# Kernel optimization log

Hardware: AMD Instinct MI355X
Metric: run time of the kernel (lower is better)

## Reference

```python
import jax, jax.numpy as jnp
import numpy as np
import math

D_MODEL = 1024
N_HEADS = 16
D_K = D_MODEL // N_HEADS
HIDDEN = 4096
R_SOFTPLUS_0 = 1.442695041
EPS = 1e-6


def setup_inputs() -> dict:
    key = jax.random.key(0)
    ks = jax.random.split(key, 16)
    B, S = 4, 2048
    s = 0.02
    inp = {
        "inputs": jax.random.normal(ks[0], (B, S, D_MODEL), jnp.float32),
        "mask": jnp.zeros((1, 1, S, S), jnp.float32),
        # RmsNorm (direct_scale=True -> init 1.0)
        "rms_scale": jnp.ones((D_MODEL,), jnp.float32),
        # attention projections (torch Linear: y = x @ W.T + b)
        "Wq": jax.random.normal(ks[1], (D_MODEL, D_MODEL), jnp.float32) * s,
        "bq": jnp.zeros((D_MODEL,), jnp.float32),
        "Wk": jax.random.normal(ks[2], (D_MODEL, D_MODEL), jnp.float32) * s,
        "bk": jnp.zeros((D_MODEL,), jnp.float32),
        "Wv": jax.random.normal(ks[3], (D_MODEL, D_MODEL), jnp.float32) * s,
        "bv": jnp.zeros((D_MODEL,), jnp.float32),
        "per_dim_scale": jnp.zeros((D_K,), jnp.float32),
        "Wpost": jax.random.normal(ks[4], (D_MODEL, D_MODEL), jnp.float32) * s,
        "bpost": jnp.zeros((D_MODEL,), jnp.float32),
        # FFN LayerNorm (direct_scale=False -> scale param init 0, effective 1+scale)
        "ln_scale": jnp.zeros((D_MODEL,), jnp.float32),
        "ln_bias": jnp.zeros((D_MODEL,), jnp.float32),
        "W1": jax.random.normal(ks[5], (HIDDEN, D_MODEL), jnp.float32) * s,
        "b1": jnp.zeros((HIDDEN,), jnp.float32),
        "W2": jax.random.normal(ks[6], (D_MODEL, HIDDEN), jnp.float32) * s,
        "b2": jnp.zeros((D_MODEL,), jnp.float32),
    }
    return inp


def _rms_norm(x, scale):
    ms = jnp.mean(x * x, axis=-1, keepdims=True)
    return x * jax.lax.rsqrt(ms + EPS) * scale


def _layer_norm(x, scale, bias):
    mean = jnp.mean(x, axis=-1, keepdims=True)
    var = jnp.mean((x - mean) ** 2, axis=-1, keepdims=True)
    return (x - mean) * jax.lax.rsqrt(var + EPS) * (1.0 + scale) + bias


def reference(inputs, mask, rms_scale, Wq, bq, Wk, bk, Wv, bv, per_dim_scale,
              Wpost, bpost, ln_scale, ln_bias, W1, b1, W2, b2):
    B, S, _ = inputs.shape
    x = _rms_norm(inputs, rms_scale)
    # projections -> [B, H, S, Dk]
    def split_heads(t):
        return t.reshape(B, S, N_HEADS, D_K).transpose(0, 2, 1, 3)
    q = split_heads(x @ Wq.T + bq)
    k = split_heads(x @ Wk.T + bk)
    v = split_heads(x @ Wv.T + bv)
    # PerDimScale: (r_softplus_0 / sqrt(d_k)) * softplus(param)
    scale = (R_SOFTPLUS_0 / math.sqrt(D_K)) * jax.nn.softplus(per_dim_scale)
    q = q * scale
    attn = jnp.einsum("bhqd,bhkd->bhqk", q, k) + mask
    attn = jax.nn.softmax(attn, axis=-1)
    out = jnp.einsum("bhqk,bhkd->bhqd", attn, v)
    out = out.transpose(0, 2, 1, 3).reshape(B, S, D_MODEL)
    attn_out = out @ Wpost.T + bpost
    h = attn_out + inputs  # residual (dropout=0)
    # FeedForward with pre-LayerNorm and residual
    y = _layer_norm(h, ln_scale, ln_bias)
    y = jax.nn.relu(y @ W1.T + b1)
    y = y @ W2.T + b2
    return y + h
```

## Files before the change

### kernel.cpp

```cpp
#include <hip/hip_runtime.h>
#include <hip/hip_bf16.h>

typedef unsigned short u16;
typedef __attribute__((ext_vector_type(8))) short short8;
typedef __attribute__((ext_vector_type(4))) float floatx4;

#define R_PDS 0.18033688f
#define LOG2E 1.4426950408889634f

__device__ __forceinline__ float bf2f(u16 u) {
    union { float f; unsigned int i; } c; c.i = ((unsigned int)u) << 16; return c.f;
}
__device__ __forceinline__ u16 f2b(float f) {
    union { float f; unsigned int i; } c; c.f = f;
    unsigned int r = c.i + 0x7fffu + ((c.i >> 16) & 1u);
    return (u16)(r >> 16);
}
__device__ __forceinline__ unsigned int pk2(float a, float b) {
    __hip_bfloat162 h = __float22bfloat162_rn(float2{a, b});
    unsigned int u; __builtin_memcpy(&u, &h, 4); return u;
}

__device__ __forceinline__ void async16(const u16* g, u16* l) {
    __builtin_amdgcn_global_load_lds(
        (const __attribute__((address_space(1))) unsigned int*)g,
        (__attribute__((address_space(3))) unsigned int*)l, 16, 0, 0);
}

__global__ __launch_bounds__(256) void f2b_all_k(const float* __restrict__ Wq, const float* __restrict__ Wk,
                                                 const float* __restrict__ Wv, const float* __restrict__ Wp,
                                                 const float* __restrict__ W1, const float* __restrict__ W2,
                                                 u16* __restrict__ Wqkvb, u16* __restrict__ Wpb,
                                                 u16* __restrict__ W1b,  u16* __restrict__ W2b,
                                                 int* flag) {
    int bid = blockIdx.x;
    if (bid == 0 && threadIdx.x == 0) *flag = 0;
    const float* src; u16* dst; int off;
    if      (bid < 1024) { src = Wq; dst = Wqkvb;                off = bid; }
    else if (bid < 2048) { src = Wk; dst = Wqkvb + 1024 * 1024;  off = bid - 1024; }
    else if (bid < 3072) { src = Wv; dst = Wqkvb + 2048 * 1024;  off = bid - 2048; }
    else if (bid < 4096) { src = Wp; dst = Wpb;                  off = bid - 3072; }
    else if (bid < 8192) { src = W1; dst = W1b;                  off = bid - 4096; }
    else                 { src = W2; dst = W2b;                  off = bid - 8192; }
    int i = off * 256 + threadIdx.x;
    float4 v = ((const float4*)src)[i];
    uint2 w; w.x = pk2(v.x, v.y); w.y = pk2(v.z, v.w);
    ((uint2*)dst)[i] = w;
}

__global__ __launch_bounds__(256) void mask_any_k(const float* __restrict__ mask, int* flag) {
    int i = blockIdx.x * 256 + threadIdx.x;
    uint4 u = ((const uint4*)mask)[i];
    unsigned int v = (u.x | u.y | u.z | u.w) & 0x7fffffffu;
    if (v) atomicOr(flag, 1);
}

__global__ __launch_bounds__(256) void rmsnorm_k(const float* __restrict__ in,
                                                 const float* __restrict__ gscale,
                                                 u16* __restrict__ out) {
    int row = blockIdx.x;
    int t = threadIdx.x, lane = t & 63, wave = t >> 6;
    const float* x = in + (size_t)row * 1024;
    float4 v = *(const float4*)(x + t * 4);
    float ss = v.x*v.x + v.y*v.y + v.z*v.z + v.w*v.w;
    for (int o = 1; o < 64; o <<= 1) ss += __shfl_xor(ss, o, 64);
    __shared__ float red[4];
    if (lane == 0) red[wave] = ss;
    __syncthreads();
    float tot = red[0] + red[1] + red[2] + red[3];
    float inv = rsqrtf(tot * (1.0f / 1024.0f) + 1e-6f);
    float4 s = *(const float4*)(gscale + t * 4);
    uint2 w;
    w.x = pk2(v.x * inv * s.x, v.y * inv * s.y);
    w.y = pk2(v.z * inv * s.z, v.w * inv * s.w);
    *(uint2*)(out + (size_t)row * 1024 + t * 4) = w;
}

__global__ __launch_bounds__(256) void layernorm_k(const u16* __restrict__ in,
                                                   const float* __restrict__ gs,
                                                   const float* __restrict__ gb,
                                                   u16* __restrict__ out) {
    int row = blockIdx.x;
    int t = threadIdx.x, lane = t & 63, wave = t >> 6;
    const u16* x = in + (size_t)row * 1024;
    uint2 u = *(const uint2*)(x + t * 4);
    float v0 = bf2f((u16)(u.x & 0xffff)), v1 = bf2f((u16)(u.x >> 16));
    float v2 = bf2f((u16)(u.y & 0xffff)), v3 = bf2f((u16)(u.y >> 16));
    float s1 = v0 + v1 + v2 + v3;
    float s2 = v0*v0 + v1*v1 + v2*v2 + v3*v3;
    for (int o = 1; o < 64; o <<= 1) { s1 += __shfl_xor(s1, o, 64); s2 += __shfl_xor(s2, o, 64); }
    __shared__ float r1[4], r2[4];
    if (lane == 0) { r1[wave] = s1; r2[wave] = s2; }
    __syncthreads();
    float mean = (r1[0] + r1[1] + r1[2] + r1[3]) * (1.0f / 1024.0f);
    float var  = (r2[0] + r2[1] + r2[2] + r2[3]) * (1.0f / 1024.0f) - mean * mean;
    var = fmaxf(var, 0.0f);
    float inv = rsqrtf(var + 1e-6f);
    float4 sc = *(const float4*)(gs + t * 4);
    float4 bb = *(const float4*)(gb + t * 4);
    uint2 w;
    w.x = pk2((v0 - mean) * inv * (1.0f + sc.x) + bb.x,
              (v1 - mean) * inv * (1.0f + sc.y) + bb.y);
    w.y = pk2((v2 - mean) * inv * (1.0f + sc.z) + bb.z,
              (v3 - mean) * inv * (1.0f + sc.w) + bb.w);
    *(uint2*)(out + (size_t)row * 1024 + t * 4) = w;
}

__device__ __forceinline__ void xcd_swizzle(int& bx, int& by) {
    int gx = gridDim.x, nwg = gx * gridDim.y;
    int lin = blockIdx.y * gx + blockIdx.x;
    int swz = (lin & 7) * (nwg >> 3) + (lin >> 3);
    bx = swz % gx; by = swz / gx;
}

__device__ __forceinline__ void gemm8_core(const u16* __restrict__ A, const u16* __restrict__ B,
                                           int K, int NG, int m0, int n0,
                                           u16* lds, floatx4 (&acc)[8][4]) {
    const int t = threadIdx.x, wave = t >> 6, lane = t & 63;
    const int quad = lane >> 4, ln = lane & 15;
    const int wave_m = wave >> 2, wave_n = wave & 3;

    const int rowS = t >> 3;
    const int srcb = ((t & 7) * 16) ^ (((t >> 3) & 7) << 4);
    const u16* Ab = A + (size_t)(m0 + rowS) * K + (srcb >> 1);
    const u16* Bb = B + (size_t)(n0 + rowS) * K + (srcb >> 1);
    const size_t rstep = (size_t)64 * K;
    const size_t hstep = (size_t)128 * K;
    const int ldw = wave * 512;

    #define STAGE_A8(buf, h, kt) do { \
        u16* _l = lds + (buf) * 32768 + (h) * 8192 + ldw; \
        const u16* _g = Ab + (size_t)(h) * hstep + (kt); \
        async16(_g, _l); async16(_g + rstep, _l + 4096); } while (0)
    #define STAGE_B8(buf, h, kt) do { \
        u16* _l = lds + (buf) * 32768 + 16384 + (h) * 8192 + ldw; \
        const u16* _g = Bb + (size_t)(h) * hstep + (kt); \
        async16(_g, _l); async16(_g + rstep, _l + 4096); } while (0)

    #define RD8(base, lr, ks) \
        (*(const short8*)((base) + (lr) * 64 + ((((ks) * 64 + quad * 16) ^ (((lr) & 7) << 4)) >> 1)))

    STAGE_B8(0, 0, 0); STAGE_B8(0, 1, 0);
    STAGE_A8(0, 0, 0); STAGE_A8(0, 1, 0);
    if (NG > 1) {
        STAGE_B8(1, 0, 64); STAGE_B8(1, 1, 64);
        asm volatile("s_waitcnt vmcnt(4)" ::: "memory");
    } else {
        asm volatile("s_waitcnt vmcnt(0)" ::: "memory");
    }
    __builtin_amdgcn_s_barrier();

    for (int g = 0; g < NG; ++g) {
        const int cur = g & 1;
        const u16* aH = lds + cur * 32768 + wave_m * 8192;
        const u16* bH = lds + cur * 32768 + 16384 + (wave_n >> 1) * 8192;
        const int lrB = (wave_n & 1) * 64;
        short8 bf[4][2];
        #pragma unroll
        for (int q = 0; q < 4; ++q) {
            short8 af[2][2];
            #pragma unroll
            for (int mt = 0; mt < 2; ++mt)
                #pragma unroll
                for (int ks = 0; ks < 2; ++ks)
                    af[mt][ks] = RD8(aH, q * 32 + mt * 16 + ln, ks);
            if (q == 0) {
                #pragma unroll
                for (int nt = 0; nt < 4; ++nt)
                    #pragma unroll
                    for (int ks = 0; ks < 2; ++ks)
                        bf[nt][ks] = RD8(bH, lrB + nt * 16 + ln, ks);
            }
            if (q == 0 && g + 1 < NG) STAGE_A8(cur ^ 1, 0, (g + 1) * 64);
            if (q == 1 && g + 1 < NG) STAGE_A8(cur ^ 1, 1, (g + 1) * 64);
            if (q == 2 && g + 2 < NG) STAGE_B8(cur, 0, (g + 2) * 64);
            if (q == 3 && g + 2 < NG) STAGE_B8(cur, 1, (g + 2) * 64);
            __builtin_amdgcn_s_barrier();
            asm volatile("s_waitcnt lgkmcnt(0)" ::: "memory");
            __builtin_amdgcn_sched_barrier(0);
            __builtin_amdgcn_s_setprio(1);
            #pragma unroll
            for (int ks = 0; ks < 2; ++ks)
                #pragma unroll
                for (int mt = 0; mt < 2; ++mt)
                    #pragma unroll
                    for (int nt = 0; nt < 4; ++nt)
                        acc[q * 2 + mt][nt] = __builtin_amdgcn_mfma_f32_16x16x32_bf16(
                            af[mt][ks], bf[nt][ks], acc[q * 2 + mt][nt], 0, 0, 0);
            __builtin_amdgcn_s_setprio(0);
            __builtin_amdgcn_sched_barrier(0);
            if (q == 3 && g + 1 < NG) {
                if (g + 2 < NG) asm volatile("s_waitcnt vmcnt(4)" ::: "memory");
                else            asm volatile("s_waitcnt vmcnt(0)" ::: "memory");
            }
            __builtin_amdgcn_s_barrier();
        }
    }
    #undef STAGE_A8
    #undef STAGE_B8
    #undef RD8
}

__device__ __forceinline__ void gemm8h_core(const u16* __restrict__ A, const u16* __restrict__ B,
                                            int K, int NG, int m0, int n0,
                                            u16* lds, floatx4 (&acc)[4][4]) {
    const int t = threadIdx.x, wave = t >> 6, lane = t & 63;
    const int quad = lane >> 4, ln = lane & 15;
    const int wm = (wave >> 2) * 64, wn = (wave & 3) * 64;

    const int rowS = t >> 3;
    const int srcb = ((t & 7) * 16) ^ (((t >> 3) & 7) << 4);
    const u16* Ab = A + (size_t)(m0 + rowS) * K + (srcb >> 1);
    const u16* Bb = B + (size_t)(n0 + rowS) * K + (srcb >> 1);
    const size_t hstep = (size_t)64 * K;
    const int ldw = wave * 512;

    #define STAGE_AH(buf, h, kt) \
        async16(Ab + (size_t)(h) * hstep + (kt), lds + (buf) * 24576 + (h) * 4096 + ldw)
    #define STAGE_BH(buf, h, kt) \
        async16(Bb + (size_t)(h) * hstep + (kt), lds + (buf) * 24576 + 8192 + (h) * 4096 + ldw)
    #define RD8H(base, lr, ks) \
        (*(const short8*)((base) + (lr) * 64 + ((((ks) * 64 + quad * 16) ^ (((lr) & 7) << 4)) >> 1)))

    STAGE_BH(0, 0, 0); STAGE_BH(0, 1, 0); STAGE_BH(0, 2, 0); STAGE_BH(0, 3, 0);
    STAGE_AH(0, 0, 0); STAGE_AH(0, 1, 0);
    if (NG > 1) {
        STAGE_BH(1, 0, 64); STAGE_BH(1, 1, 64); STAGE_BH(1, 2, 64); STAGE_BH(1, 3, 64);
        asm volatile("s_waitcnt vmcnt(4)" ::: "memory");
    } else {
        asm volatile("s_waitcnt vmcnt(0)" ::: "memory");
    }
    __builtin_amdgcn_s_barrier();

    for (int g = 0; g < NG; ++g) {
        const int cur = g & 1;
        const u16* aB = lds + cur * 24576;
        const u16* bB = lds + cur * 24576 + 8192;
        short8 bf[4][2];
        #pragma unroll
        for (int q = 0; q < 2; ++q) {
            short8 af[2][2];
            #pragma unroll
            for (int mt = 0; mt < 2; ++mt)
                #pragma unroll
                for (int ks = 0; ks < 2; ++ks)
                    af[mt][ks] = RD8H(aB, wm + (q * 2 + mt) * 16 + ln, ks);
            if (q == 0) {
                #pragma unroll
                for (int nt = 0; nt < 4; ++nt)
                    #pragma unroll
                    for (int ks = 0; ks < 2; ++ks)
                        bf[nt][ks] = RD8H(bB, wn + nt * 16 + ln, ks);
            }
            if (q == 0 && g + 1 < NG) {
                STAGE_AH(cur ^ 1, 0, (g + 1) * 64); STAGE_AH(cur ^ 1, 1, (g + 1) * 64);
            }
            if (q == 1 && g + 2 < NG) {
                STAGE_BH(cur, 0, (g + 2) * 64); STAGE_BH(cur, 1, (g + 2) * 64);
                STAGE_BH(cur, 2, (g + 2) * 64); STAGE_BH(cur, 3, (g + 2) * 64);
            }
            __builtin_amdgcn_s_barrier();
            asm volatile("s_waitcnt lgkmcnt(0)" ::: "memory");
            __builtin_amdgcn_sched_barrier(0);
            __builtin_amdgcn_s_setprio(1);
            #pragma unroll
            for (int ks = 0; ks < 2; ++ks)
                #pragma unroll
                for (int mt = 0; mt < 2; ++mt)
                    #pragma unroll
                    for (int nt = 0; nt < 4; ++nt)
                        acc[q * 2 + mt][nt] = __builtin_amdgcn_mfma_f32_16x16x32_bf16(
                            af[mt][ks], bf[nt][ks], acc[q * 2 + mt][nt], 0, 0, 0);
            __builtin_amdgcn_s_setprio(0);
            __builtin_amdgcn_sched_barrier(0);
            if (q == 1 && g + 1 < NG) {
                if (g + 2 < NG) asm volatile("s_waitcnt vmcnt(4)" ::: "memory");
                else            asm volatile("s_waitcnt vmcnt(0)" ::: "memory");
            }
            __builtin_amdgcn_s_barrier();
        }
    }
    #undef STAGE_AH
    #undef STAGE_BH
    #undef RD8H
}

template <int EPI, bool OUTF32, bool RESF32>
__global__ __launch_bounds__(512, 2) void gemm8_bt_k(const u16* __restrict__ A,
                                                     const u16* __restrict__ B,
                                                     const float* __restrict__ bias,
                                                     const void* __restrict__ res,
                                                     void* __restrict__ Cv,
                                                     int M, int N, int K) {
    __shared__ __align__(16) u16 lds[65536];
    int bx, by; xcd_swizzle(bx, by);
    const int m0 = by * 256, n0 = bx * 256;
    const int t = threadIdx.x, wave = t >> 6, lane = t & 63;
    const int quad = lane >> 4, ln = lane & 15;
    const int wm = (wave >> 2) * 128, wn = (wave & 3) * 64;

    floatx4 acc[8][4];
    #pragma unroll
    for (int mf = 0; mf < 8; mf++)
        #pragma unroll
        for (int nf = 0; nf < 4; nf++) acc[mf][nf] = (floatx4)0.0f;

    gemm8_core(A, B, K, K >> 6, m0, n0, lds, acc);

    #pragma unroll
    for (int nf = 0; nf < 4; nf++) {
        int col = n0 + wn + nf * 16 + ln;
        float bv = bias[col];
        #pragma unroll
        for (int mf = 0; mf < 8; mf++) {
            int row = m0 + wm + mf * 16 + quad * 4;
            #pragma unroll
            for (int r = 0; r < 4; r++) {
                float v = acc[mf][nf][r] + bv;
                if (EPI == 1) v = fmaxf(v, 0.0f);
                if (EPI == 2) {
                    if (RESF32) v += ((const float*)res)[(size_t)(row + r) * N + col];
                    else        v += bf2f(((const u16*)res)[(size_t)(row + r) * N + col]);
                }
                if (OUTF32) ((float*)Cv)[(size_t)(row + r) * N + col] = v;
                else        ((u16*)Cv)[(size_t)(row + r) * N + col] = f2b(v);
            }
        }
    }
}

template <int EPI, bool OUTF32, bool RESF32>
__global__ __launch_bounds__(512, 2) void gemm8h_bt_k(const u16* __restrict__ A,
                                                      const u16* __restrict__ B,
                                                      const float* __restrict__ bias,
                                                      const void* __restrict__ res,
                                                      void* __restrict__ Cv,
                                                      int M, int N, int K) {
    __shared__ __align__(16) u16 lds[49152];
    int bx, by; xcd_swizzle(bx, by);
    const int m0 = by * 128, n0 = bx * 256;
    const int t = threadIdx.x, wave = t >> 6, lane = t & 63;
    const int quad = lane >> 4, ln = lane & 15;
    const int wm = (wave >> 2) * 64, wn = (wave & 3) * 64;

    floatx4 acc[4][4];
    #pragma unroll
    for (int mf = 0; mf < 4; mf++)
        #pragma unroll
        for (int nf = 0; nf < 4; nf++) acc[mf][nf] = (floatx4)0.0f;

    gemm8h_core(A, B, K, K >> 6, m0, n0, lds, acc);

    #pragma unroll
    for (int nf = 0; nf < 4; nf++) {
        int col = n0 + wn + nf * 16 + ln;
        float bv = bias[col];
        #pragma unroll
        for (int mf = 0; mf < 4; mf++) {
            int row = m0 + wm + mf * 16 + quad * 4;
            #pragma unroll
            for (int r = 0; r < 4; r++) {
                float v = acc[mf][nf][r] + bv;
                if (EPI == 1) v = fmaxf(v, 0.0f);
                if (EPI == 2) {
                    if (RESF32) v += ((const float*)res)[(size_t)(row + r) * N + col];
                    else        v += bf2f(((const u16*)res)[(size_t)(row + r) * N + col]);
                }
                if (OUTF32) ((float*)Cv)[(size_t)(row + r) * N + col] = v;
                else        ((u16*)Cv)[(size_t)(row + r) * N + col] = f2b(v);
            }
        }
    }
}

__global__ __launch_bounds__(512, 2) void gemm8h_qkv_k(const u16* __restrict__ A,
                                                       const u16* __restrict__ B,
                                                       const float* __restrict__ bq,
                                                       const float* __restrict__ bk,
                                                       const float* __restrict__ bv,
                                                       const float* __restrict__ pds,
                                                       u16* __restrict__ C) {
    const int K = 1024, N = 3072;
    __shared__ __align__(16) u16 lds[49152];
    int bx, by; xcd_swizzle(bx, by);
    const int m0 = by * 128, n0 = bx * 256;
    const int t = threadIdx.x, wave = t >> 6, lane = t & 63;
    const int quad = lane >> 4, ln = lane & 15;
    const int wm = (wave >> 2) * 64, wn = (wave & 3) * 64;

    floatx4 acc[4][4];
    #pragma unroll
    for (int mf = 0; mf < 4; mf++)
        #pragma unroll
        for (int nf = 0; nf < 4; nf++) acc[mf][nf] = (floatx4)0.0f;

    gemm8h_core(A, B, K, K >> 6, m0, n0, lds, acc);

    #pragma unroll
    for (int nf = 0; nf < 4; nf++) {
        int col = n0 + wn + nf * 16 + ln;
        float bv_, sc = 1.0f;
        if (col < 1024) {
            bv_ = bq[col];
            float xp = pds[col & 63];
            float sp = (xp > 20.0f) ? xp : log1pf(__expf(xp));
            sc = R_PDS * sp * LOG2E;
        } else if (col < 2048) bv_ = bk[col - 1024];
        else                   bv_ = bv[col - 2048];
        #pragma unroll
        for (int mf = 0; mf < 4; mf++) {
            int row = m0 + wm + mf * 16 + quad * 4;
            #pragma unroll
            for (int r = 0; r < 4; r++)
                C[(size_t)(row + r) * N + col] = f2b((acc[mf][nf][r] + bv_) * sc);
        }
    }
}

__global__ __launch_bounds__(256) void transpose_v_k(const u16* __restrict__ qkv, u16* __restrict__ vT) {
    __shared__ u16 tile[64][65];
    int st = blockIdx.x, bh = blockIdx.y;
    int b = bh >> 4, h = bh & 15;
    const u16* vb = qkv + (size_t)(b * 2048 + st * 64) * 3072 + 2048 + h * 64;
    int t = threadIdx.x;
    for (int i = t; i < 4096; i += 256) {
        int s = i >> 6, d = i & 63;
        tile[s][d] = vb[(size_t)s * 3072 + d];
    }
    __syncthreads();
    u16* ob = vT + (size_t)bh * 131072 + st * 64;
    for (int i = t; i < 4096; i += 256) {
        int d = i >> 6, s = i & 63;
        ob[(size_t)d * 2048 + s] = tile[s][d];
    }
}

__global__ __launch_bounds__(256, 4) void attn_k(const u16* __restrict__ qkv,
                                                 const u16* __restrict__ vT,
                                                 const float* __restrict__ mask,
                                                 const int* __restrict__ flag,
                                                 u16* __restrict__ o) {
    __shared__ __align__(16) u16 Ksh[4096];
    __shared__ __align__(16) u16 Vsh[4096];
    __shared__ __align__(16) u16 Ps[4096];

    const int t = threadIdx.x, wave = t >> 6, lane = t & 63;
    const int quad = lane >> 4, ln = lane & 15;
    const int lin = blockIdx.y * 16 + blockIdx.x;
    const int qt = (lin >> 3) & 15;
    const int bh = ((lin & 7) << 3) | (lin >> 7);
    const int b = bh >> 4, h = bh & 15;
    const int q0 = qt * 128;
    const int wm = wave * 32;

    const u16* qb = qkv + (size_t)(b * 2048 + q0) * 3072 + h * 64;
    short8 qf[2][2];
    #pragma unroll
    for (int mt = 0; mt < 2; mt++)
        #pragma unroll
        for (int ks = 0; ks < 2; ks++)
            qf[mt][ks] = *(const short8*)(qb + (size_t)(wm + mt * 16 + ln) * 3072 + ks * 32 + quad * 8);

    const int swzK = (ln & 7) << 4;
    const int swzP = (ln & 3) << 4;
    const int o_kA0 = ln * 128 + ((quad * 16) ^ swzK);
    const int o_kA1 = ln * 128 + ((64 + quad * 16) ^ swzK);
    const int o_pv  = ln * 64 + ((quad * 16) ^ swzP);
    const int o_pw0 = wave * 2048 + ln * 64 + ((quad * 8) ^ swzP);
    const int o_pw1 = wave * 2048 + ln * 64 + ((32 + quad * 8) ^ swzP);
    const int o_pr  = wave * 2048 + o_pv;

    #define RD8AT(arr, byteoff) (*(const short8*)((const char*)(arr) + (byteoff)))

    const int rK = t >> 3, sK = (((t & 7) ^ (rK & 7))) * 8;
    const int rV = t >> 2, sV = (((t & 3) ^ (rV & 3))) * 8;
    const u16* kgp = qkv + (size_t)(b * 2048) * 3072 + 1024 + h * 64 + (size_t)rK * 3072 + sK;
    const u16* vgp = vT + (size_t)bh * 131072 + (size_t)rV * 2048 + sV;
    const size_t KADV = (size_t)32 * 3072;

    #define STAGE(c, tile) do { \
        async16(kgp + (size_t)(tile) * KADV, Ksh + (c) * 2048 + t * 8); \
        async16(vgp + (size_t)(tile) * 32,   Vsh + (c) * 2048 + t * 8); } while (0)

    short8 ones_f;
    #pragma unroll
    for (int i = 0; i < 8; i++) ones_f[i] = (short)0x3F80;

    floatx4 acc_o[2][4], acc_l[2];
    #pragma unroll
    for (int mt = 0; mt < 2; mt++) {
        acc_l[mt] = (floatx4)0.0f;
        #pragma unroll
        for (int dt = 0; dt < 4; dt++) acc_o[mt][dt] = (floatx4)0.0f;
    }

    const int mflag = *flag;
    int kvbase = 0;

    STAGE(0, 0);
    STAGE(1, 1);
    asm volatile("s_waitcnt vmcnt(2)" ::: "memory");
    __builtin_amdgcn_s_barrier();

    #define COMPUTE(BUF) do {                                                              \
                           \
        _Pragma("unroll")                                                                  \
        for (int nt = 0; nt < 2; nt++) {                                                   \
            short8 kf0 = RD8AT(Ksh, (BUF) * 4096 + nt * 2048 + o_kA0);                     \
            short8 kf1 = RD8AT(Ksh, (BUF) * 4096 + nt * 2048 + o_kA1);                     \
            floatx4 sa0 = (floatx4)0.0f, sa1 = (floatx4)0.0f;                              \
            sa0 = __builtin_amdgcn_mfma_f32_16x16x32_bf16(kf0, qf[0][0], sa0, 0, 0, 0);    \
            sa0 = __builtin_amdgcn_mfma_f32_16x16x32_bf16(kf1, qf[0][1], sa0, 0, 0, 0);    \
            sa1 = __builtin_amdgcn_mfma_f32_16x16x32_bf16(kf0, qf[1][0], sa1, 0, 0, 0);    \
            sa1 = __builtin_amdgcn_mfma_f32_16x16x32_bf16(kf1, qf[1][1], sa1, 0, 0, 0);    \
            if (mflag) {                                                                   \
                _Pragma("unroll")                                                          \
                for (int r = 0; r < 4; r++) {                                              \
                    int kc = kvbase + nt * 16 + quad * 4 + r;                              \
                    sa0[r] += mask[(size_t)(q0 + wm + ln) * 2048 + kc] * LOG2E;            \
                    sa1[r] += mask[(size_t)(q0 + wm + 16 + ln) * 2048 + kc] * LOG2E;       \
                }                                                                          \
            }                                                                              \
            {                                                                              \
                uint2 w;                                                                   \
                w.x = pk2(__builtin_amdgcn_exp2f(fminf(sa0[0], 80.0f)),                    \
                          __builtin_amdgcn_exp2f(fminf(sa0[1], 80.0f)));                   \
                w.y = pk2(__builtin_amdgcn_exp2f(fminf(sa0[2], 80.0f)),                    \
                          __builtin_amdgcn_exp2f(fminf(sa0[3], 80.0f)));                   \
                *(uint2*)((char*)Ps + (nt ? o_pw1 : o_pw0)) = w;                           \
            }                                                                              \
            {                                                                              \
                uint2 w;                                                                   \
                w.x = pk2(__builtin_amdgcn_exp2f(fminf(sa1[0], 80.0f)),                    \
                          __builtin_amdgcn_exp2f(fminf(sa1[1], 80.0f)));                   \
                w.y = pk2(__builtin_amdgcn_exp2f(fminf(sa1[2], 80.0f)),                    \
                          __builtin_amdgcn_exp2f(fminf(sa1[3], 80.0f)));                   \
                *(uint2*)((char*)Ps + (nt ? o_pw1 : o_pw0) + 1024) = w;                    \
            }                                                                              \
        }                                                                                  \
                                     \
        {                                                                                  \
            short8 vf0 = RD8AT(Vsh, (BUF) * 4096 + 0 * 1024 + o_pv);                       \
            short8 vf1 = RD8AT(Vsh, (BUF) * 4096 + 1 * 1024 + o_pv);                       \
            short8 vf2 = RD8AT(Vsh, (BUF) * 4096 + 2 * 1024 + o_pv);                       \
            short8 vf3 = RD8AT(Vsh, (BUF) * 4096 + 3 * 1024 + o_pv);                       \
            _Pragma("unroll")                                                              \
            for (int mt = 0; mt < 2; mt++) {                                               \
                short8 a = RD8AT(Ps, o_pr + mt * 1024);                                    \
                acc_l[mt] = __builtin_amdgcn_mfma_f32_16x16x32_bf16(a, ones_f, acc_l[mt], 0, 0, 0); \
                acc_o[mt][0] = __builtin_amdgcn_mfma_f32_16x16x32_bf16(a, vf0, acc_o[mt][0], 0, 0, 0); \
                acc_o[mt][1] = __builtin_amdgcn_mfma_f32_16x16x32_bf16(a, vf1, acc_o[mt][1], 0, 0, 0); \
                acc_o[mt][2] = __builtin_amdgcn_mfma_f32_16x16x32_bf16(a, vf2, acc_o[mt][2], 0, 0, 0); \
                acc_o[mt][3] = __builtin_amdgcn_mfma_f32_16x16x32_bf16(a, vf3, acc_o[mt][3], 0, 0, 0); \
            }                                                                              \
        }                                                                                  \
    } while (0)

    #pragma unroll 1
    for (int it = 0; it < 32; ++it) {
        COMPUTE(0);
        __builtin_amdgcn_s_barrier();
        if (it < 31) {
            STAGE(0, 2 * it + 2);
            asm volatile("s_waitcnt vmcnt(2)" ::: "memory");
        } else {
            asm volatile("s_waitcnt vmcnt(0)" ::: "memory");
        }
        __builtin_amdgcn_s_barrier();
        kvbase += 32;
        COMPUTE(1);
        __builtin_amdgcn_s_barrier();
        if (it < 31) {
            STAGE(1, 2 * it + 3);
            asm volatile("s_waitcnt vmcnt(2)" ::: "memory");
        } else {
            asm volatile("s_waitcnt vmcnt(0)" ::: "memory");
        }
        __builtin_amdgcn_s_barrier();
        kvbase += 32;
    }
    #undef COMPUTE
    #undef STAGE
    #undef RD8AT

    u16* ob = o + (size_t)(b * 2048 + q0) * 1024 + h * 64;
    #pragma unroll
    for (int mt = 0; mt < 2; mt++) {
        #pragma unroll
        for (int r = 0; r < 4; r++) {
            float inv = 1.0f / acc_l[mt][r];
            int row = wm + mt * 16 + quad * 4 + r;
            #pragma unroll
            for (int dt = 0; dt < 4; dt++)
                ob[(size_t)row * 1024 + dt * 16 + ln] = f2b(acc_o[mt][dt][r] * inv);
        }
    }
}

extern "C" void kernel_launch(void* const* d_in, const int* in_sizes, int n_in,
                              void* d_out, int out_size, void* d_ws, size_t ws_size,
                              hipStream_t stream) {
    const float* inp    = (const float*)d_in[0];
    const float* mask   = (const float*)d_in[1];
    const float* rms_s  = (const float*)d_in[2];
    const float* Wq     = (const float*)d_in[3];
    const float* bq     = (const float*)d_in[4];
    const float* Wk     = (const float*)d_in[5];
    const float* bk     = (const float*)d_in[6];
    const float* Wv     = (const float*)d_in[7];
    const float* bv     = (const float*)d_in[8];
    const float* pds    = (const float*)d_in[9];
    const float* Wpost  = (const float*)d_in[10];
    const float* bpost  = (const float*)d_in[11];
    const float* ln_s   = (const float*)d_in[12];
    const float* ln_b   = (const float*)d_in[13];
    const float* W1     = (const float*)d_in[14];
    const float* b1     = (const float*)d_in[15];
    const float* W2     = (const float*)d_in[16];
    const float* b2     = (const float*)d_in[17];
    float* out = (float*)d_out;

    char* w = (char*)d_ws;
    const size_t MB = 1u << 20;
    u16* W1b   = (u16*)(w + 0 * MB);
    u16* W2b   = (u16*)(w + 8 * MB);
    u16* qkv   = (u16*)(w + 16 * MB);
    u16* x     = (u16*)(w + 64 * MB);
    u16* o     = (u16*)(w + 64 * MB);
    u16* Wqkvb = (u16*)(w + 80 * MB);
    u16* Wpb   = (u16*)(w + 86 * MB);
    u16* yln   = (u16*)(w + 80 * MB);
    u16* vT    = (u16*)(w + 96 * MB);
    u16* hb    = (u16*)(w + 96 * MB);
    u16* f1    = (u16*)(w + 16 * MB);
    int* flag  = (int*)(w + 112 * MB);

    f2b_all_k<<<12288, 256, 0, stream>>>(Wq, Wk, Wv, Wpost, W1, W2, Wqkvb, Wpb, W1b, W2b, flag);
    mask_any_k<<<4096, 256, 0, stream>>>(mask, flag);

    rmsnorm_k<<<8192, 256, 0, stream>>>(inp, rms_s, x);

    gemm8h_qkv_k<<<dim3(12, 64), 512, 0, stream>>>(x, Wqkvb, bq, bk, bv, pds, qkv);

    transpose_v_k<<<dim3(32, 64), 256, 0, stream>>>(qkv, vT);

    attn_k<<<dim3(16, 64), 256, 0, stream>>>(qkv, vT, mask, flag, o);

    gemm8h_bt_k<2, false, true><<<dim3(4, 64), 512, 0, stream>>>(o, Wpb, bpost, inp, hb, 8192, 1024, 1024);

    layernorm_k<<<8192, 256, 0, stream>>>(hb, ln_s, ln_b, yln);

    gemm8_bt_k<1, false, true><<<dim3(16, 32), 512, 0, stream>>>(yln, W1b, b1, nullptr, f1, 8192, 4096, 1024);
    gemm8h_bt_k<2, true, false><<<dim3(4, 64), 512, 0, stream>>>(f1, W2b, b2, hb, out, 8192, 1024, 4096);
}
```

Baseline: 518.7 us.

## Fuse mask check into RMSNorm, write V transposed from QKV GEMM, widen attention KV tile

Merges the mask-nonzero scan into the RMSNorm launch as extra blocks. The QKV GEMM epilogue now writes V directly into the transposed per-head layout, which removes the separate transpose kernel and its round trip through memory. The attention kernel's KV tile grows from 32 to 64 per stage, with larger LDS buffers and occupancy lowered from 4 to 3 blocks per CU. This means fewer iterations and barriers, at the cost of occupancy and scattered 8-byte V stores.

```diff
diff --git a/kernel.cpp b/kernel.cpp
--- a/kernel.cpp
+++ b/kernel.cpp
@@ -48,23 +48,25 @@
     ((uint2*)dst)[i] = w;
 }
 
-__global__ __launch_bounds__(256) void mask_any_k(const float* __restrict__ mask, int* flag) {
-    int i = blockIdx.x * 256 + threadIdx.x;
-    uint4 u = ((const uint4*)mask)[i];
-    unsigned int v = (u.x | u.y | u.z | u.w) & 0x7fffffffu;
-    if (v) atomicOr(flag, 1);
-}
-
-__global__ __launch_bounds__(256) void rmsnorm_k(const float* __restrict__ in,
-                                                 const float* __restrict__ gscale,
-                                                 u16* __restrict__ out) {
-    int row = blockIdx.x;
+__global__ __launch_bounds__(256) void rms_mask_k(const float* __restrict__ in,
+                                                  const float* __restrict__ gscale,
+                                                  u16* __restrict__ out,
+                                                  const float* __restrict__ mask,
+                                                  int* flag) {
+    __shared__ float red[4];
+    int bid = blockIdx.x;
     int t = threadIdx.x, lane = t & 63, wave = t >> 6;
-    const float* x = in + (size_t)row * 1024;
+    if (bid >= 8192) {
+        int i = (bid - 8192) * 256 + t;
+        uint4 u = ((const uint4*)mask)[i];
+        unsigned int v = (u.x | u.y | u.z | u.w) & 0x7fffffffu;
+        if (v) atomicOr(flag, 1);
+        return;
+    }
+    const float* x = in + (size_t)bid * 1024;
     float4 v = *(const float4*)(x + t * 4);
     float ss = v.x*v.x + v.y*v.y + v.z*v.z + v.w*v.w;
     for (int o = 1; o < 64; o <<= 1) ss += __shfl_xor(ss, o, 64);
-    __shared__ float red[4];
     if (lane == 0) red[wave] = ss;
     __syncthreads();
     float tot = red[0] + red[1] + red[2] + red[3];
@@ -73,7 +75,7 @@
     uint2 w;
     w.x = pk2(v.x * inv * s.x, v.y * inv * s.y);
     w.y = pk2(v.z * inv * s.z, v.w * inv * s.w);
-    *(uint2*)(out + (size_t)row * 1024 + t * 4) = w;
+    *(uint2*)(out + (size_t)bid * 1024 + t * 4) = w;
 }
 
 __global__ __launch_bounds__(256) void layernorm_k(const u16* __restrict__ in,
@@ -379,7 +381,8 @@
                                                        const float* __restrict__ bk,
                                                        const float* __restrict__ bv,
                                                        const float* __restrict__ pds,
-                                                       u16* __restrict__ C) {
+                                                       u16* __restrict__ C,
+                                                       u16* __restrict__ vTout) {
     const int K = 1024, N = 3072;
     __shared__ __align__(16) u16 lds[49152];
     int bx, by; xcd_swizzle(bx, by);
@@ -399,50 +402,49 @@
     #pragma unroll
     for (int nf = 0; nf < 4; nf++) {
         int col = n0 + wn + nf * 16 + ln;
-        float bv_, sc = 1.0f;
-        if (col < 1024) {
-            bv_ = bq[col];
-            float xp = pds[col & 63];
-            float sp = (xp > 20.0f) ? xp : log1pf(__expf(xp));
-            sc = R_PDS * sp * LOG2E;
-        } else if (col < 2048) bv_ = bk[col - 1024];
-        else                   bv_ = bv[col - 2048];
-        #pragma unroll
-        for (int mf = 0; mf < 4; mf++) {
-            int row = m0 + wm + mf * 16 + quad * 4;
-            #pragma unroll
-            for (int r = 0; r < 4; r++)
-                C[(size_t)(row + r) * N + col] = f2b((acc[mf][nf][r] + bv_) * sc);
-        }
-    }
-}
-
-__global__ __launch_bounds__(256) void transpose_v_k(const u16* __restrict__ qkv, u16* __restrict__ vT) {
-    __shared__ u16 tile[64][65];
-    int st = blockIdx.x, bh = blockIdx.y;
-    int b = bh >> 4, h = bh & 15;
-    const u16* vb = qkv + (size_t)(b * 2048 + st * 64) * 3072 + 2048 + h * 64;
-    int t = threadIdx.x;
-    for (int i = t; i < 4096; i += 256) {
-        int s = i >> 6, d = i & 63;
-        tile[s][d] = vb[(size_t)s * 3072 + d];
-    }
-    __syncthreads();
-    u16* ob = vT + (size_t)bh * 131072 + st * 64;
-    for (int i = t; i < 4096; i += 256) {
-        int d = i >> 6, s = i & 63;
-        ob[(size_t)d * 2048 + s] = tile[s][d];
-    }
-}
-
-__global__ __launch_bounds__(256, 4) void attn_k(const u16* __restrict__ qkv,
+        if (col < 2048) {
+            float bv_, sc = 1.0f;
+            if (col < 1024) {
+                bv_ = bq[col];
+                float xp = pds[col & 63];
+                float sp = (xp > 20.0f) ? xp : log1pf(__expf(xp));
+                sc = R_PDS * sp * LOG2E;
+            } else bv_ = bk[col - 1024];
+            #pragma unroll
+            for (int mf = 0; mf < 4; mf++) {
+                int row = m0 + wm + mf * 16 + quad * 4;
+                #pragma unroll
+                for (int r = 0; r < 4; r++)
+                    C[(size_t)(row + r) * N + col] = f2b((acc[mf][nf][r] + bv_) * sc);
+            }
+        } else {
+            float bv_ = bv[col - 2048];
+            int hh = (col - 2048) >> 6, dd = (col - 2048) & 63;
+            #pragma unroll
+            for (int mf = 0; mf < 4; mf++) {
+                int row = m0 + wm + mf * 16 + quad * 4;
+                int bb = row >> 11, ss = row & 2047;
+                u16 u0 = f2b(acc[mf][nf][0] + bv_);
+                u16 u1 = f2b(acc[mf][nf][1] + bv_);
+                u16 u2 = f2b(acc[mf][nf][2] + bv_);
+                u16 u3 = f2b(acc[mf][nf][3] + bv_);
+                uint2 w;
+                w.x = (unsigned int)u0 | ((unsigned int)u1 << 16);
+                w.y = (unsigned int)u2 | ((unsigned int)u3 << 16);
+                *(uint2*)(vTout + (size_t)(bb * 16 + hh) * 131072 + (size_t)dd * 2048 + ss) = w;
+            }
+        }
+    }
+}
+
+__global__ __launch_bounds__(256, 3) void attn_k(const u16* __restrict__ qkv,
                                                  const u16* __restrict__ vT,
                                                  const float* __restrict__ mask,
                                                  const int* __restrict__ flag,
                                                  u16* __restrict__ o) {
-    __shared__ __align__(16) u16 Ksh[4096];
-    __shared__ __align__(16) u16 Vsh[4096];
-    __shared__ __align__(16) u16 Ps[4096];
+    __shared__ __align__(16) u16 Ksh[8192];
+    __shared__ __align__(16) u16 Vsh[8192];
+    __shared__ __align__(16) u16 Ps[8192];
 
     const int t = threadIdx.x, wave = t >> 6, lane = t & 63;
     const int quad = lane >> 4, ln = lane & 15;
@@ -461,26 +463,28 @@
         for (int ks = 0; ks < 2; ks++)
             qf[mt][ks] = *(const short8*)(qb + (size_t)(wm + mt * 16 + ln) * 3072 + ks * 32 + quad * 8);
 
-    const int swzK = (ln & 7) << 4;
-    const int swzP = (ln & 3) << 4;
-    const int o_kA0 = ln * 128 + ((quad * 16) ^ swzK);
-    const int o_kA1 = ln * 128 + ((64 + quad * 16) ^ swzK);
-    const int o_pv  = ln * 64 + ((quad * 16) ^ swzP);
-    const int o_pw0 = wave * 2048 + ln * 64 + ((quad * 8) ^ swzP);
-    const int o_pw1 = wave * 2048 + ln * 64 + ((32 + quad * 8) ^ swzP);
-    const int o_pr  = wave * 2048 + o_pv;
+    const int swz = (ln & 7) << 4;
+    const int o_f0 = ln * 128 + ((quad * 16) ^ swz);
+    const int o_f1 = ln * 128 + ((64 + quad * 16) ^ swz);
+    const int o_q0 = (wm + ln) * 128 + ((quad * 16) ^ swz);
+    const int o_q1 = (wm + ln) * 128 + ((64 + quad * 16) ^ swz);
+    int o_p[4];
+    #pragma unroll
+    for (int nt = 0; nt < 4; nt++)
+        o_p[nt] = (wm + ln) * 128 + ((nt * 32 + quad * 8) ^ swz);
 
     #define RD8AT(arr, byteoff) (*(const short8*)((const char*)(arr) + (byteoff)))
 
-    const int rK = t >> 3, sK = (((t & 7) ^ (rK & 7))) * 8;
-    const int rV = t >> 2, sV = (((t & 3) ^ (rV & 3))) * 8;
-    const u16* kgp = qkv + (size_t)(b * 2048) * 3072 + 1024 + h * 64 + (size_t)rK * 3072 + sK;
-    const u16* vgp = vT + (size_t)bh * 131072 + (size_t)rV * 2048 + sV;
-    const size_t KADV = (size_t)32 * 3072;
-
-    #define STAGE(c, tile) do { \
-        async16(kgp + (size_t)(tile) * KADV, Ksh + (c) * 2048 + t * 8); \
-        async16(vgp + (size_t)(tile) * 32,   Vsh + (c) * 2048 + t * 8); } while (0)
+    const int rS = t >> 3;
+    const int cS = ((t & 7) ^ (rS & 7)) * 8;
+    const u16* kg = qkv + (size_t)(b * 2048) * 3072 + 1024 + h * 64 + (size_t)rS * 3072 + cS;
+    const u16* vg = vT + (size_t)bh * 131072 + (size_t)rS * 2048 + cS;
+
+    #define STAGE(c, kv0_) do { \
+        async16(kg + (size_t)(kv0_) * 3072,        Ksh + (c) * 4096 + t * 8); \
+        async16(kg + (size_t)((kv0_) + 32) * 3072, Ksh + (c) * 4096 + 2048 + t * 8); \
+        async16(vg + (kv0_),                       Vsh + (c) * 4096 + t * 8); \
+        async16(vg + (size_t)32 * 2048 + (kv0_),   Vsh + (c) * 4096 + 2048 + t * 8); } while (0)
 
     short8 ones_f;
     #pragma unroll
@@ -498,16 +502,15 @@
     int kvbase = 0;
 
     STAGE(0, 0);
-    STAGE(1, 1);
-    asm volatile("s_waitcnt vmcnt(2)" ::: "memory");
+    STAGE(1, 64);
+    asm volatile("s_waitcnt vmcnt(4)" ::: "memory");
     __builtin_amdgcn_s_barrier();
 
     #define COMPUTE(BUF) do {                                                              \
-                           \
         _Pragma("unroll")                                                                  \
-        for (int nt = 0; nt < 2; nt++) {                                                   \
-            short8 kf0 = RD8AT(Ksh, (BUF) * 4096 + nt * 2048 + o_kA0);                     \
-            short8 kf1 = RD8AT(Ksh, (BUF) * 4096 + nt * 2048 + o_kA1);                     \
+        for (int nt = 0; nt < 4; nt++) {                                                   \
+            short8 kf0 = RD8AT(Ksh, (BUF) * 8192 + nt * 2048 + o_f0);                      \
+            short8 kf1 = RD8AT(Ksh, (BUF) * 8192 + nt * 2048 + o_f1);                      \
             floatx4 sa0 = (floatx4)0.0f, sa1 = (floatx4)0.0f;                              \
             sa0 = __builtin_amdgcn_mfma_f32_16x16x32_bf16(kf0, qf[0][0], sa0, 0, 0, 0);    \
             sa0 = __builtin_amdgcn_mfma_f32_16x16x32_bf16(kf1, qf[0][1], sa0, 0, 0, 0);    \
@@ -527,7 +530,7 @@
                           __builtin_amdgcn_exp2f(fminf(sa0[1], 80.0f)));                   \
                 w.y = pk2(__builtin_amdgcn_exp2f(fminf(sa0[2], 80.0f)),                    \
                           __builtin_amdgcn_exp2f(fminf(sa0[3], 80.0f)));                   \
-                *(uint2*)((char*)Ps + (nt ? o_pw1 : o_pw0)) = w;                           \
+                *(uint2*)((char*)Ps + o_p[nt]) = w;                                        \
             }                                                                              \
             {                                                                              \
                 uint2 w;                                                                   \
@@ -535,49 +538,48 @@
                           __builtin_amdgcn_exp2f(fminf(sa1[1], 80.0f)));                   \
                 w.y = pk2(__builtin_amdgcn_exp2f(fminf(sa1[2], 80.0f)),                    \
                           __builtin_amdgcn_exp2f(fminf(sa1[3], 80.0f)));                   \
-                *(uint2*)((char*)Ps + (nt ? o_pw1 : o_pw0) + 1024) = w;                    \
+                *(uint2*)((char*)Ps + o_p[nt] + 2048) = w;                                 \
             }                                                                              \
         }                                                                                  \
-                                     \
-        {                                                                                  \
-            short8 vf0 = RD8AT(Vsh, (BUF) * 4096 + 0 * 1024 + o_pv);                       \
-            short8 vf1 = RD8AT(Vsh, (BUF) * 4096 + 1 * 1024 + o_pv);                       \
-            short8 vf2 = RD8AT(Vsh, (BUF) * 4096 + 2 * 1024 + o_pv);                       \
-            short8 vf3 = RD8AT(Vsh, (BUF) * 4096 + 3 * 1024 + o_pv);                       \
+        _Pragma("unroll")                                                                  \
+        for (int ks = 0; ks < 2; ks++) {                                                   \
+            const int of = ks ? o_f1 : o_f0;                                               \
+            const int oq = ks ? o_q1 : o_q0;                                               \
+            short8 a0 = RD8AT(Ps, oq);                                                     \
+            short8 a1 = RD8AT(Ps, oq + 2048);                                              \
+            acc_l[0] = __builtin_amdgcn_mfma_f32_16x16x32_bf16(a0, ones_f, acc_l[0], 0, 0, 0); \
+            acc_l[1] = __builtin_amdgcn_mfma_f32_16x16x32_bf16(a1, ones_f, acc_l[1], 0, 0, 0); \
             _Pragma("unroll")                                                              \
-            for (int mt = 0; mt < 2; mt++) {                                               \
-                short8 a = RD8AT(Ps, o_pr + mt * 1024);                                    \
-                acc_l[mt] = __builtin_amdgcn_mfma_f32_16x16x32_bf16(a, ones_f, acc_l[mt], 0, 0, 0); \
-                acc_o[mt][0] = __builtin_amdgcn_mfma_f32_16x16x32_bf16(a, vf0, acc_o[mt][0], 0, 0, 0); \
-                acc_o[mt][1] = __builtin_amdgcn_mfma_f32_16x16x32_bf16(a, vf1, acc_o[mt][1], 0, 0, 0); \
-                acc_o[mt][2] = __builtin_amdgcn_mfma_f32_16x16x32_bf16(a, vf2, acc_o[mt][2], 0, 0, 0); \
-                acc_o[mt][3] = __builtin_amdgcn_mfma_f32_16x16x32_bf16(a, vf3, acc_o[mt][3], 0, 0, 0); \
+            for (int dt = 0; dt < 4; dt++) {                                               \
+                short8 vf = RD8AT(Vsh, (BUF) * 8192 + dt * 2048 + of);                     \
+                acc_o[0][dt] = __builtin_amdgcn_mfma_f32_16x16x32_bf16(a0, vf, acc_o[0][dt], 0, 0, 0); \
+                acc_o[1][dt] = __builtin_amdgcn_mfma_f32_16x16x32_bf16(a1, vf, acc_o[1][dt], 0, 0, 0); \
             }                                                                              \
         }                                                                                  \
     } while (0)
 
     #pragma unroll 1
-    for (int it = 0; it < 32; ++it) {
+    for (int it = 0; it < 16; ++it) {
         COMPUTE(0);
         __builtin_amdgcn_s_barrier();
-        if (it < 31) {
-            STAGE(0, 2 * it + 2);
-            asm volatile("s_waitcnt vmcnt(2)" ::: "memory");
+        if (it < 15) {
+            STAGE(0, it * 128 + 128);
+            asm volatile("s_waitcnt vmcnt(4)" ::: "memory");
         } else {
             asm volatile("s_waitcnt vmcnt(0)" ::: "memory");
         }
         __builtin_amdgcn_s_barrier();
-        kvbase += 32;
+        kvbase += 64;
         COMPUTE(1);
         __builtin_amdgcn_s_barrier();
-        if (it < 31) {
-            STAGE(1, 2 * it + 3);
-            asm volatile("s_waitcnt vmcnt(2)" ::: "memory");
+        if (it < 15) {
+            STAGE(1, it * 128 + 192);
+            asm volatile("s_waitcnt vmcnt(4)" ::: "memory");
         } else {
             asm volatile("s_waitcnt vmcnt(0)" ::: "memory");
         }
         __builtin_amdgcn_s_barrier();
-        kvbase += 32;
+        kvbase += 64;
     }
     #undef COMPUTE
     #undef STAGE
@@ -636,13 +638,10 @@
     int* flag  = (int*)(w + 112 * MB);
 
     f2b_all_k<<<12288, 256, 0, stream>>>(Wq, Wk, Wv, Wpost, W1, W2, Wqkvb, Wpb, W1b, W2b, flag);
-    mask_any_k<<<4096, 256, 0, stream>>>(mask, flag);
-
-    rmsnorm_k<<<8192, 256, 0, stream>>>(inp, rms_s, x);
-
-    gemm8h_qkv_k<<<dim3(12, 64), 512, 0, stream>>>(x, Wqkvb, bq, bk, bv, pds, qkv);
-
-    transpose_v_k<<<dim3(32, 64), 256, 0, stream>>>(qkv, vT);
+
+    rms_mask_k<<<12288, 256, 0, stream>>>(inp, rms_s, x, mask, flag);
+
+    gemm8h_qkv_k<<<dim3(12, 64), 512, 0, stream>>>(x, Wqkvb, bq, bk, bv, pds, qkv, vT);
 
     attn_k<<<dim3(16, 64), 256, 0, stream>>>(qkv, vT, mask, flag, o);
 
```

Result: no change. 520.4 us (+0.3%).
